# Kernel optimization log

Hardware: AMD Instinct MI355X
Metric: run time of the kernel (lower is better)

Reference implementation:

```python
import jax, jax.numpy as jnp
import numpy as np

N = 100000        # nodes
E = 1600000       # edges (avg degree 16)
IN_CH = 128
HID = 64
NUM_CLASSES = 40
LAYERS = 15
DT = 0.1
JACOBI_STEPS = 2


def setup_inputs() -> dict:
    key = jax.random.key(0)
    ks = jax.random.split(key, 8)
    x = jax.random.normal(ks[0], (N, IN_CH), dtype=jnp.float32)
    edge_index = jax.random.randint(ks[1], (2, E), 0, N, dtype=jnp.int32)
    s = 1.0 / np.sqrt(IN_CH)
    W_lx = jax.random.normal(ks[2], (IN_CH, HID), dtype=jnp.float32) * s
    b_lx = jnp.zeros((HID,), dtype=jnp.float32)
    W_ly = jax.random.normal(ks[3], (IN_CH, HID), dtype=jnp.float32) * s
    b_ly = jnp.zeros((HID,), dtype=jnp.float32)
    taus = jnp.full((LAYERS,), 0.7, dtype=jnp.float32)
    logit_scale = jnp.asarray(2.5, dtype=jnp.float32)
    W_ro = jax.random.normal(ks[4], (HID, NUM_CLASSES), dtype=jnp.float32) * (1.0 / np.sqrt(HID))
    b_ro = jnp.zeros((NUM_CLASSES,), dtype=jnp.float32)
    return {"x": x, "W_lx": W_lx, "b_lx": b_lx, "W_ly": W_ly, "b_ly": b_ly,
            "taus": taus, "logit_scale": logit_scale, "W_ro": W_ro, "b_ro": b_ro,
            "edge_index": edge_index}


def reference(x, W_lx, b_lx, W_ly, b_ly, taus, logit_scale, W_ro, b_ro, edge_index):
    # Eval mode: dropout is identity. y0_mode='ones' so lift_y is unused.
    src, dst = edge_index[0], edge_index[1]
    # symmetric normalization D^-1/2 A D^-1/2 from edge list
    deg = jax.ops.segment_sum(jnp.ones((E,), dtype=x.dtype), dst, num_segments=N)
    dinv = jax.lax.rsqrt(jnp.maximum(deg, 1.0))
    enorm = dinv[src] * dinv[dst]              # [E]

    def agg(Z):                                 # A_hat @ Z  via gather/scatter
        return jax.ops.segment_sum(enorm[:, None] * Z[src], dst, num_segments=N)

    X0 = jnp.tanh(x @ W_lx + b_lx)              # [N, HID]
    Y0 = jnp.ones_like(X0)
    h = jnp.concatenate([X0, Y0], axis=-1)      # [N, 2*HID]

    for l in range(LAYERS):
        X, Y = h[:, :HID], h[:, HID:]
        # Lotka-Volterra reaction terms
        fX = X * (1.0 - Y)
        fY = Y * (X - 1.0)
        rhs = jnp.concatenate([X + DT * fX, Y + DT * fY], axis=-1)
        # semi-implicit diffusion: ((1+dt)I - dt*A_hat) Z = rhs, Jacobi iterations
        Z = rhs
        for _ in range(JACOBI_STEPS):
            Z = (rhs + DT * agg(Z)) / (1.0 + DT)
        tau = jax.nn.sigmoid(taus[l])
        h = (1.0 - tau) * h + tau * Z

    Xout = h[:, :HID]
    return (logit_scale * Xout) @ W_ro + b_ro   # [N, NUM_CLASSES]
```

## Files before the change

### kernel.cpp

```cpp
#include <hip/hip_runtime.h>

#define DT_C   0.1f
#define INV1P  0.9090909090909091f


__device__ __forceinline__ unsigned bf16rne(float f) {
  unsigned b = __float_as_uint(f);
  return (b + 0x7fffu + ((b >> 16) & 1u)) >> 16;
}
__device__ __forceinline__ unsigned packbf(float x, float y) {
  return bf16rne(x) | (bf16rne(y) << 16);
}


#if __has_builtin(__builtin_amdgcn_cvt_pk_fp8_f32) && __has_builtin(__builtin_amdgcn_cvt_pk_f32_fp8)
typedef float vf2 __attribute__((ext_vector_type(2)));
__device__ __forceinline__ unsigned pk4_fp8(float a, float b, float c, float d) {
  int v = __builtin_amdgcn_cvt_pk_fp8_f32(a, b, 0, false);
  v = __builtin_amdgcn_cvt_pk_fp8_f32(c, d, v, true);
  return (unsigned)v;
}
__device__ __forceinline__ void unpk4_fp8(unsigned v, float& a, float& b, float& c, float& d) {
  vf2 lo = __builtin_amdgcn_cvt_pk_f32_fp8((int)v, false);
  vf2 hi = __builtin_amdgcn_cvt_pk_f32_fp8((int)v, true);
  a = lo[0]; b = lo[1]; c = hi[0]; d = hi[1];
}
#else
__device__ __forceinline__ unsigned enc8(float f) {
  unsigned u = __float_as_uint(f);
  unsigned mag = u & 0x7fffffffu;
  if (mag > 0x43E00000u) mag = 0x43E00000u;
  unsigned r = mag + 0x7FFFFu + ((mag >> 20) & 1u);
  int e8 = (int)(r >> 23) - 120;
  unsigned code = 0;
  if (e8 > 0) code = ((unsigned)(e8 > 15 ? 15 : e8) << 3) | ((r >> 20) & 7u);
  return code | ((u >> 24) & 0x80u);
}
__device__ __forceinline__ float dec8(unsigned c) {
  unsigned e = (c >> 3) & 15u, m = c & 7u, s = (c & 0x80u) << 24;
  if (e == 0) return __uint_as_float(s);
  return __uint_as_float(s | ((e + 120u) << 23) | (m << 20));
}
__device__ __forceinline__ unsigned pk4_fp8(float a, float b, float c, float d) {
  return enc8(a) | (enc8(b) << 8) | (enc8(c) << 16) | (enc8(d) << 24);
}
__device__ __forceinline__ void unpk4_fp8(unsigned v, float& a, float& b, float& c, float& d) {
  a = dec8(v & 0xffu); b = dec8((v >> 8) & 0xffu);
  c = dec8((v >> 16) & 0xffu); d = dec8(v >> 24);
}
#endif


__global__ __launch_bounds__(256) void k_deg(const int* __restrict__ dst,
                                             int* __restrict__ deg, int e) {
  int i = blockIdx.x * 256 + threadIdx.x;
  if (i < e) atomicAdd(&deg[dst[i]], 1);
}

__global__ __launch_bounds__(256) void k_dinv(const int* __restrict__ deg,
                                              float* __restrict__ dinv, int n) {
  int i = blockIdx.x * 256 + threadIdx.x;
  if (i < n) {
    float d = (float)deg[i];
    dinv[i] = rsqrtf(fmaxf(d, 1.0f));
  }
}

__global__ __launch_bounds__(1024) void k_scanA(const int* __restrict__ deg,
                                                int* __restrict__ rowptr,
                                                int* __restrict__ bsum, int n) {
  __shared__ int sm[1024];
  int t = threadIdx.x;
  int i = blockIdx.x * 1024 + t;
  int v = (i < n) ? deg[i] : 0;
  sm[t] = v;
  __syncthreads();
  for (int off = 1; off < 1024; off <<= 1) {
    int u = (t >= off) ? sm[t - off] : 0;
    __syncthreads();
    sm[t] += u;
    __syncthreads();
  }
  if (i < n) rowptr[i] = sm[t] - v;
  if (t == 1023) bsum[blockIdx.x] = sm[t];
}

__global__ __launch_bounds__(1024) void k_scanB(int* __restrict__ bsum, int g) {
  __shared__ int sm[1024];
  int t = threadIdx.x;
  int v = (t < g) ? bsum[t] : 0;
  sm[t] = v;
  __syncthreads();
  for (int off = 1; off < 1024; off <<= 1) {
    int u = (t >= off) ? sm[t - off] : 0;
    __syncthreads();
    sm[t] += u;
    __syncthreads();
  }
  if (t < g) bsum[t] = sm[t] - v;
}

__global__ __launch_bounds__(1024) void k_scanC(int* __restrict__ rowptr,
                                                const int* __restrict__ bsum,
                                                int n, int etot) {
  int i = blockIdx.x * 1024 + threadIdx.x;
  if (i < n) rowptr[i] += bsum[blockIdx.x];
  if (i == 0) rowptr[n] = etot;
}

__global__ __launch_bounds__(256) void k_fill(const int* __restrict__ src,
                                              const int* __restrict__ dst,
                                              const int* __restrict__ rowptr,
                                              int* __restrict__ deg,
                                              const float* __restrict__ dinv,
                                              unsigned* __restrict__ csr, int e) {
  int i = blockIdx.x * 256 + threadIdx.x;
  if (i >= e) return;
  int s = src[i], d = dst[i];
  int pos = rowptr[d] + atomicSub(&deg[d], 1) - 1;
  unsigned wb = __float_as_uint(dinv[s] * dinv[d]);
  wb = (wb + 0x10000u) & 0xFFFE0000u;
  csr[pos] = wb | (unsigned)s;
}


__global__ __launch_bounds__(256) void k_gemm_in(const float* __restrict__ x,
                                                 const float* __restrict__ Wlx,
                                                 const float* __restrict__ blx,
                                                 unsigned* __restrict__ h_b,
                                                 unsigned* __restrict__ rhs8,
                                                 int n, int ntiles) {
  __shared__ float xs[16 * 128];
  int t = threadIdx.x;
  int lane = t & 63;
  int wib  = t >> 6;
  unsigned wp[64];
#pragma unroll
  for (int j = 0; j < 64; ++j)
    wp[j] = packbf(Wlx[(2 * j) * 64 + lane], Wlx[(2 * j + 1) * 64 + lane]);
  float bl = blx[lane];

  for (int tile = blockIdx.x; tile < ntiles; tile += gridDim.x) {
    int base = tile * 16;
    __syncthreads();
    for (int v = t; v < 512; v += 256) {
      long idx = (long)base * 128 + v * 4;
      float4 val = {0.f, 0.f, 0.f, 0.f};
      if (idx < (long)n * 128) val = *(const float4*)(x + idx);
      *(float4*)(xs + v * 4) = val;
    }
    __syncthreads();
    for (int r = 0; r < 4; ++r) {
      int row = base + wib * 4 + r;
      if (row < n) {
        const float* xr = &xs[(wib * 4 + r) * 128];
        float acc = bl;
#pragma unroll
        for (int j = 0; j < 32; ++j) {
          float4 xv = *(const float4*)(xr + j * 4);
          unsigned p0 = wp[2 * j], p1 = wp[2 * j + 1];
          acc = fmaf(xv.x, __uint_as_float(p0 << 16),         acc);
          acc = fmaf(xv.y, __uint_as_float(p0 & 0xffff0000u), acc);
          acc = fmaf(xv.z, __uint_as_float(p1 << 16),         acc);
          acc = fmaf(xv.w, __uint_as_float(p1 & 0xffff0000u), acc);
        }
        float X0 = tanhf(acc);
        float a = __shfl(X0, (2 * lane) & 63);
        float b = __shfl(X0, (2 * lane + 1) & 63);
        unsigned hw = (lane < 32) ? packbf(a, b) : 0x3f803f80u;
        h_b[(size_t)row * 64 + lane] = hw;
        int b4 = (lane < 16) ? 4 * lane : 4 * (lane - 16);
        float v0 = __shfl(X0, (b4 + 0) & 63);
        float v1 = __shfl(X0, (b4 + 1) & 63);
        float v2 = __shfl(X0, (b4 + 2) & 63);
        float v3 = __shfl(X0, (b4 + 3) & 63);
        if (lane >= 16) {
          v0 = 1.f + DT_C * (v0 - 1.f);
          v1 = 1.f + DT_C * (v1 - 1.f);
          v2 = 1.f + DT_C * (v2 - 1.f);
          v3 = 1.f + DT_C * (v3 - 1.f);
        }
        unsigned pw = pk4_fp8(v0, v1, v2, v3);
        if (lane < 32) rhs8[(size_t)row * 32 + lane] = pw;
      }
    }
  }
}


__device__ __forceinline__ void rch_from_h(const unsigned hw[4], int q,
                                           float hv[8], float rch[8]) {
#pragma unroll
  for (int i = 0; i < 4; ++i) {
    hv[2 * i]     = __uint_as_float(hw[i] << 16);
    hv[2 * i + 1] = __uint_as_float(hw[i] & 0xffff0000u);
  }
  float pv[8];
#pragma unroll
  for (int i = 0; i < 8; ++i) pv[i] = __shfl_xor(hv[i], 8);
  bool isX = (q < 8);
#pragma unroll
  for (int i = 0; i < 8; ++i)
    rch[i] = isX ? hv[i] + DT_C * hv[i] * (1.0f - pv[i])
                 : hv[i] + DT_C * hv[i] * (pv[i] - 1.0f);
}

__device__ __forceinline__ void gather8(const unsigned* __restrict__ Zb8,
                                        const unsigned* __restrict__ csr,
                                        int beg, int end, int g, int q,
                                        float acc[8]) {
#pragma unroll
  for (int i = 0; i < 8; ++i) acc[i] = 0.f;
  int last = end - 1;
  const uint2* Z2 = (const uint2*)Zb8;
  for (int e0 = beg; e0 < end; e0 += 16) {
    unsigned c[4]; float wk[4]; uint2 u[4];
#pragma unroll
    for (int k = 0; k < 4; ++k) {
      int idx = e0 + 4 * k + g;
      int ic  = (idx < end) ? idx : last;
      c[k]  = csr[ic];
      wk[k] = (idx < end) ? __uint_as_float(c[k] & 0xFFFE0000u) : 0.f;
    }
#pragma unroll
    for (int k = 0; k < 4; ++k)
      u[k] = Z2[(size_t)(c[k] & 0x1FFFFu) * 16 + q];
#pragma unroll
    for (int k = 0; k < 4; ++k) {
      float f0, f1, f2, f3, f4, f5, f6, f7;
      unpk4_fp8(u[k].x, f0, f1, f2, f3);
      unpk4_fp8(u[k].y, f4, f5, f6, f7);
      acc[0] = fmaf(wk[k], f0, acc[0]);
      acc[1] = fmaf(wk[k], f1, acc[1]);
      acc[2] = fmaf(wk[k], f2, acc[2]);
      acc[3] = fmaf(wk[k], f3, acc[3]);
      acc[4] = fmaf(wk[k], f4, acc[4]);
      acc[5] = fmaf(wk[k], f5, acc[5]);
      acc[6] = fmaf(wk[k], f6, acc[6]);
      acc[7] = fmaf(wk[k], f7, acc[7]);
    }
  }
#pragma unroll
  for (int i = 0; i < 8; ++i) {
    acc[i] += __shfl_xor(acc[i], 16);
    acc[i] += __shfl_xor(acc[i], 32);
  }
}


__global__ __launch_bounds__(256) void k_aggA(const unsigned* __restrict__ rhs8,
                                              unsigned* __restrict__ Z18,
                                              const unsigned* __restrict__ h_b,
                                              const int* __restrict__ rowptr,
                                              const unsigned* __restrict__ csr, int n) {
  int node = __builtin_amdgcn_readfirstlane((blockIdx.x * 256 + threadIdx.x) >> 6);
  if (node >= n) return;
  int lane = threadIdx.x & 63;
  int g = lane >> 4, q = lane & 15;
  int beg = __builtin_amdgcn_readfirstlane(rowptr[node]);
  int end = __builtin_amdgcn_readfirstlane(rowptr[node + 1]);

  uint4 hb = *((const uint4*)(h_b + (size_t)node * 64) + q);
  unsigned hw[4] = {hb.x, hb.y, hb.z, hb.w};
  float hv[8], rch[8];
  rch_from_h(hw, q, hv, rch);

  float acc[8];
  gather8(rhs8, csr, beg, end, g, q, acc);

  float z[8];
#pragma unroll
  for (int i = 0; i < 8; ++i) z[i] = (rch[i] + DT_C * acc[i]) * INV1P;
  if (g == 0) {
    uint2 o;
    o.x = pk4_fp8(z[0], z[1], z[2], z[3]);
    o.y = pk4_fp8(z[4], z[5], z[6], z[7]);
    ((uint2*)Z18)[(size_t)node * 16 + q] = o;
  }
}


__global__ __launch_bounds__(256) void k_aggB(const unsigned* __restrict__ Z18,
                                              unsigned* __restrict__ rhs8,
                                              unsigned* __restrict__ h_b,
                                              const int* __restrict__ rowptr,
                                              const unsigned* __restrict__ csr,
                                              const float* __restrict__ taus,
                                              int layer, int n) {
  int node = __builtin_amdgcn_readfirstlane((blockIdx.x * 256 + threadIdx.x) >> 6);
  if (node >= n) return;
  int lane = threadIdx.x & 63;
  int g = lane >> 4, q = lane & 15;
  int beg = __builtin_amdgcn_readfirstlane(rowptr[node]);
  int end = __builtin_amdgcn_readfirstlane(rowptr[node + 1]);

  uint4 hb = *((const uint4*)(h_b + (size_t)node * 64) + q);
  unsigned hw[4] = {hb.x, hb.y, hb.z, hb.w};
  float hv[8], rch[8];
  rch_from_h(hw, q, hv, rch);

  float acc[8];
  gather8(Z18, csr, beg, end, g, q, acc);

  float tv  = taus[layer];
  float tau = 1.0f / (1.0f + expf(-tv));
  float hnew[8];
#pragma unroll
  for (int i = 0; i < 8; ++i) {
    float z = (rch[i] + DT_C * acc[i]) * INV1P;
    hnew[i] = (1.0f - tau) * hv[i] + tau * z;
  }
  if (g == 0) {
    uint4 o;
    o.x = packbf(hnew[0], hnew[1]);
    o.y = packbf(hnew[2], hnew[3]);
    o.z = packbf(hnew[4], hnew[5]);
    o.w = packbf(hnew[6], hnew[7]);
    *((uint4*)(h_b + (size_t)node * 64) + q) = o;
  }
  float pn[8];
#pragma unroll
  for (int i = 0; i < 8; ++i) pn[i] = __shfl_xor(hnew[i], 8);
  bool isX = (q < 8);
  float rn[8];
#pragma unroll
  for (int i = 0; i < 8; ++i)
    rn[i] = isX ? hnew[i] + DT_C * hnew[i] * (1.0f - pn[i])
                : hnew[i] + DT_C * hnew[i] * (pn[i] - 1.0f);
  if (g == 0) {
    uint2 o;
    o.x = pk4_fp8(rn[0], rn[1], rn[2], rn[3]);
    o.y = pk4_fp8(rn[4], rn[5], rn[6], rn[7]);
    ((uint2*)rhs8)[(size_t)node * 16 + q] = o;
  }
}


__global__ __launch_bounds__(256) void k_gemm_out(const unsigned* __restrict__ h_b,
                                                  const float* __restrict__ Wro,
                                                  const float* __restrict__ bro,
                                                  const float* __restrict__ lscale,
                                                  float* __restrict__ out, int n) {
  __shared__ float ws[64 * 40];
  __shared__ float xs[16 * 64];
  int t = threadIdx.x;
  for (int i = t; i < 64 * 40; i += 256) ws[i] = Wro[i];
  int base = blockIdx.x * 16;
  for (int v = t; v < 512; v += 256) {
    int rr = v >> 5;
    int wq = v & 31;
    int row = base + rr;
    float a = 0.f, b = 0.f;
    if (row < n) {
      unsigned u = h_b[(size_t)row * 64 + wq];
      a = __uint_as_float(u << 16);
      b = __uint_as_float(u & 0xffff0000u);
    }
    xs[rr * 64 + 2 * wq]     = a;
    xs[rr * 64 + 2 * wq + 1] = b;
  }
  __syncthreads();
  float ls = *lscale;
  int lane = t & 63;
  int wib  = t >> 6;
  float bb = (lane < 40) ? bro[lane] : 0.f;
  for (int r = 0; r < 4; ++r) {
    int row = base + wib * 4 + r;
    if (row < n && lane < 40) {
      const float* xr = &xs[(wib * 4 + r) * 64];
      float acc = 0.f;
#pragma unroll
      for (int k = 0; k < 64; ++k) acc = fmaf(xr[k], ws[k * 40 + lane], acc);
      out[row * 40 + lane] = ls * acc + bb;
    }
  }
}


extern "C" void kernel_launch(void* const* d_in, const int* in_sizes, int n_in,
                              void* d_out, int out_size, void* d_ws, size_t ws_size,
                              hipStream_t stream) {
  const float* x     = (const float*)d_in[0];
  const float* Wlx   = (const float*)d_in[1];
  const float* blx   = (const float*)d_in[2];
  const float* taus  = (const float*)d_in[5];
  const float* lsc   = (const float*)d_in[6];
  const float* Wro   = (const float*)d_in[7];
  const float* bro   = (const float*)d_in[8];
  const int*   eidx  = (const int*)d_in[9];
  int n = in_sizes[0] / 128;
  int e = in_sizes[9] / 2;
  const int* srcp = eidx;
  const int* dstp = eidx + e;
  float* out = (float*)d_out;

  char* ws = (char*)d_ws;
  size_t off = 0;
  auto alloc = [&](size_t bytes) -> void* {
    void* p = ws + off;
    off += (bytes + 255) & ~(size_t)255;
    return p;
  };
  int*      deg     = (int*)     alloc((size_t)n * 4);
  float*    dinv    = (float*)   alloc((size_t)n * 4);
  int*      rowptr  = (int*)     alloc((size_t)(n + 1) * 4);
  int*      bsum    = (int*)     alloc(1024 * 4);
  unsigned* csr     = (unsigned*)alloc((size_t)e * 4);
  unsigned* h_b     = (unsigned*)alloc((size_t)n * 64 * 4);
  unsigned* rhs8    = (unsigned*)alloc((size_t)n * 32 * 4);
  unsigned* Z18     = (unsigned*)alloc((size_t)n * 32 * 4);
  (void)ws_size; (void)n_in; (void)out_size;

  (void)hipMemsetAsync(deg, 0, (size_t)n * 4, stream);

  int eb = (e + 255) / 256;
  int sb = (n + 1023) / 1024;
  k_deg <<<eb, 256, 0, stream>>>(dstp, deg, e);
  k_dinv<<<(n + 255) / 256, 256, 0, stream>>>(deg, dinv, n);
  k_scanA<<<sb, 1024, 0, stream>>>(deg, rowptr, bsum, n);
  k_scanB<<<1, 1024, 0, stream>>>(bsum, sb);
  k_scanC<<<sb, 1024, 0, stream>>>(rowptr, bsum, n, e);
  k_fill<<<eb, 256, 0, stream>>>(srcp, dstp, rowptr, deg, dinv, csr, e);

  int ntiles = (n + 15) / 16;
  int gb = ntiles < 2048 ? ntiles : 2048;
  k_gemm_in<<<gb, 256, 0, stream>>>(x, Wlx, blx, h_b, rhs8, n, ntiles);

  int ab = (n * 64 + 255) / 256;
  for (int l = 0; l < 15; ++l) {
    k_aggA<<<ab, 256, 0, stream>>>(rhs8, Z18, h_b, rowptr, csr, n);
    k_aggB<<<ab, 256, 0, stream>>>(Z18, rhs8, h_b, rowptr, csr, taus, l, n);
  }

  k_gemm_out<<<(n + 15) / 16, 256, 0, stream>>>(h_b, Wro, bro, lsc, out, n);
}
```

Before: 1.691 ms.

## Process two nodes per wavefront in aggregation and drop h_b read in aggA

Each wavefront now handles two adjacent CSR rows in both Jacobi aggregation kernels, interleaving their edge gathers to raise memory-level parallelism. The first Jacobi kernel takes the right-hand side from the fp8 rhs buffer instead of recomputing it from bf16 h, removing one read of the state. The input GEMM is restructured to one wave per row, using lane shuffles instead of LDS staging. Costs are more registers per thread, fewer waves, and slightly different rounding in the first Jacobi step.

```diff
diff --git a/kernel.cpp b/kernel.cpp
--- a/kernel.cpp
+++ b/kernel.cpp
@@ -128,68 +128,159 @@
                                                  const float* __restrict__ Wlx,
                                                  const float* __restrict__ blx,
                                                  unsigned* __restrict__ h_b,
-                                                 unsigned* __restrict__ rhs8,
-                                                 int n, int ntiles) {
-  __shared__ float xs[16 * 128];
-  int t = threadIdx.x;
+                                                 unsigned* __restrict__ rhs8, int n) {
+  int t = blockIdx.x * 256 + threadIdx.x;
   int lane = t & 63;
-  int wib  = t >> 6;
+  int wid  = t >> 6;
+  int nW   = (gridDim.x * 256) >> 6;
   unsigned wp[64];
 #pragma unroll
   for (int j = 0; j < 64; ++j)
     wp[j] = packbf(Wlx[(2 * j) * 64 + lane], Wlx[(2 * j + 1) * 64 + lane]);
   float bl = blx[lane];
 
-  for (int tile = blockIdx.x; tile < ntiles; tile += gridDim.x) {
-    int base = tile * 16;
-    __syncthreads();
-    for (int v = t; v < 512; v += 256) {
-      long idx = (long)base * 128 + v * 4;
-      float4 val = {0.f, 0.f, 0.f, 0.f};
-      if (idx < (long)n * 128) val = *(const float4*)(x + idx);
-      *(float4*)(xs + v * 4) = val;
-    }
-    __syncthreads();
-    for (int r = 0; r < 4; ++r) {
-      int row = base + wib * 4 + r;
-      if (row < n) {
-        const float* xr = &xs[(wib * 4 + r) * 128];
-        float acc = bl;
-#pragma unroll
-        for (int j = 0; j < 32; ++j) {
-          float4 xv = *(const float4*)(xr + j * 4);
-          unsigned p0 = wp[2 * j], p1 = wp[2 * j + 1];
-          acc = fmaf(xv.x, __uint_as_float(p0 << 16),         acc);
-          acc = fmaf(xv.y, __uint_as_float(p0 & 0xffff0000u), acc);
-          acc = fmaf(xv.z, __uint_as_float(p1 << 16),         acc);
-          acc = fmaf(xv.w, __uint_as_float(p1 & 0xffff0000u), acc);
-        }
-        float X0 = tanhf(acc);
-        float a = __shfl(X0, (2 * lane) & 63);
-        float b = __shfl(X0, (2 * lane + 1) & 63);
-        unsigned hw = (lane < 32) ? packbf(a, b) : 0x3f803f80u;
-        h_b[(size_t)row * 64 + lane] = hw;
-        int b4 = (lane < 16) ? 4 * lane : 4 * (lane - 16);
-        float v0 = __shfl(X0, (b4 + 0) & 63);
-        float v1 = __shfl(X0, (b4 + 1) & 63);
-        float v2 = __shfl(X0, (b4 + 2) & 63);
-        float v3 = __shfl(X0, (b4 + 3) & 63);
-        if (lane >= 16) {
-          v0 = 1.f + DT_C * (v0 - 1.f);
-          v1 = 1.f + DT_C * (v1 - 1.f);
-          v2 = 1.f + DT_C * (v2 - 1.f);
-          v3 = 1.f + DT_C * (v3 - 1.f);
-        }
-        unsigned pw = pk4_fp8(v0, v1, v2, v3);
-        if (lane < 32) rhs8[(size_t)row * 32 + lane] = pw;
+  for (int row = wid; row < n; row += nW) {
+    float2 xv = *(const float2*)(x + (size_t)row * 128 + 2 * lane);
+    float acc = bl;
+#pragma unroll
+    for (int k = 0; k < 64; ++k) {
+      float bx = __shfl(xv.x, k);
+      float by = __shfl(xv.y, k);
+      acc = fmaf(bx, __uint_as_float(wp[k] << 16),         acc);
+      acc = fmaf(by, __uint_as_float(wp[k] & 0xffff0000u), acc);
+    }
+    float X0 = tanhf(acc);
+    float a = __shfl(X0, (2 * lane) & 63);
+    float b = __shfl(X0, (2 * lane + 1) & 63);
+    unsigned hw = (lane < 32) ? packbf(a, b) : 0x3f803f80u;
+    h_b[(size_t)row * 64 + lane] = hw;
+    int b4 = (lane < 16) ? 4 * lane : 4 * (lane - 16);
+    float v0 = __shfl(X0, (b4 + 0) & 63);
+    float v1 = __shfl(X0, (b4 + 1) & 63);
+    float v2 = __shfl(X0, (b4 + 2) & 63);
+    float v3 = __shfl(X0, (b4 + 3) & 63);
+    if (lane >= 16) {
+      v0 = 1.f + DT_C * (v0 - 1.f);
+      v1 = 1.f + DT_C * (v1 - 1.f);
+      v2 = 1.f + DT_C * (v2 - 1.f);
+      v3 = 1.f + DT_C * (v3 - 1.f);
+    }
+    unsigned pw = pk4_fp8(v0, v1, v2, v3);
+    if (lane < 32) rhs8[(size_t)row * 32 + lane] = pw;
+  }
+}
+
+
+__device__ __forceinline__ void batch_fma(const unsigned c[4], const float wk[4],
+                                          const uint2 u[4], float acc[8]) {
+#pragma unroll
+  for (int k = 0; k < 4; ++k) {
+    float f0, f1, f2, f3, f4, f5, f6, f7;
+    unpk4_fp8(u[k].x, f0, f1, f2, f3);
+    unpk4_fp8(u[k].y, f4, f5, f6, f7);
+    acc[0] = fmaf(wk[k], f0, acc[0]);
+    acc[1] = fmaf(wk[k], f1, acc[1]);
+    acc[2] = fmaf(wk[k], f2, acc[2]);
+    acc[3] = fmaf(wk[k], f3, acc[3]);
+    acc[4] = fmaf(wk[k], f4, acc[4]);
+    acc[5] = fmaf(wk[k], f5, acc[5]);
+    acc[6] = fmaf(wk[k], f6, acc[6]);
+    acc[7] = fmaf(wk[k], f7, acc[7]);
+  }
+}
+
+
+__global__ __launch_bounds__(256) void k_aggA(const unsigned* __restrict__ rhs8,
+                                              unsigned* __restrict__ Z18,
+                                              const int* __restrict__ rowptr,
+                                              const unsigned* __restrict__ csr, int n) {
+  int pair = __builtin_amdgcn_readfirstlane((blockIdx.x * 256 + threadIdx.x) >> 6);
+  int nodeA = 2 * pair;
+  if (nodeA >= n) return;
+  int nodeB = nodeA + 1;
+  bool hasB = nodeB < n;
+  int lane = threadIdx.x & 63;
+  int g = lane >> 4, q = lane & 15;
+  int begA = __builtin_amdgcn_readfirstlane(rowptr[nodeA]);
+  int endA = __builtin_amdgcn_readfirstlane(rowptr[nodeA + 1]);
+  int begB = endA;
+  int endB = hasB ? __builtin_amdgcn_readfirstlane(rowptr[nodeB + 1]) : begB;
+
+  const uint2* Z2 = (const uint2*)rhs8;
+  uint2 ra = Z2[(size_t)nodeA * 16 + q];
+  uint2 rb = hasB ? Z2[(size_t)nodeB * 16 + q] : ra;
+
+  float accA[8] = {0, 0, 0, 0, 0, 0, 0, 0};
+  float accB[8] = {0, 0, 0, 0, 0, 0, 0, 0};
+  int lastA = endA - 1, lastB = endB - 1;
+  for (int eA = begA, eB = begB; (eA < endA) || (eB < endB); eA += 16, eB += 16) {
+    bool doA = eA < endA, doB = eB < endB;
+    unsigned cA[4], cB[4]; float wA[4], wB[4]; uint2 uA[4], uB[4];
+    if (doA) {
+#pragma unroll
+      for (int k = 0; k < 4; ++k) {
+        int idx = eA + 4 * k + g;
+        int ic  = (idx < endA) ? idx : lastA;
+        cA[k] = csr[ic];
+        wA[k] = (idx < endA) ? __uint_as_float(cA[k] & 0xFFFE0000u) : 0.f;
       }
     }
-  }
-}
-
-
-__device__ __forceinline__ void rch_from_h(const unsigned hw[4], int q,
+    if (doB) {
+#pragma unroll
+      for (int k = 0; k < 4; ++k) {
+        int idx = eB + 4 * k + g;
+        int ic  = (idx < endB) ? idx : lastB;
+        cB[k] = csr[ic];
+        wB[k] = (idx < endB) ? __uint_as_float(cB[k] & 0xFFFE0000u) : 0.f;
+      }
+    }
+    if (doA) {
+#pragma unroll
+      for (int k = 0; k < 4; ++k) uA[k] = Z2[(size_t)(cA[k] & 0x1FFFFu) * 16 + q];
+    }
+    if (doB) {
+#pragma unroll
+      for (int k = 0; k < 4; ++k) uB[k] = Z2[(size_t)(cB[k] & 0x1FFFFu) * 16 + q];
+    }
+    if (doA) batch_fma(cA, wA, uA, accA);
+    if (doB) batch_fma(cB, wB, uB, accB);
+  }
+#pragma unroll
+  for (int i = 0; i < 8; ++i) {
+    accA[i] += __shfl_xor(accA[i], 16);
+    accA[i] += __shfl_xor(accA[i], 32);
+    accB[i] += __shfl_xor(accB[i], 16);
+    accB[i] += __shfl_xor(accB[i], 32);
+  }
+  float r8[8];
+  unpk4_fp8(ra.x, r8[0], r8[1], r8[2], r8[3]);
+  unpk4_fp8(ra.y, r8[4], r8[5], r8[6], r8[7]);
+  if (g == 0) {
+    uint2 o;
+    o.x = pk4_fp8((r8[0] + DT_C * accA[0]) * INV1P, (r8[1] + DT_C * accA[1]) * INV1P,
+                  (r8[2] + DT_C * accA[2]) * INV1P, (r8[3] + DT_C * accA[3]) * INV1P);
+    o.y = pk4_fp8((r8[4] + DT_C * accA[4]) * INV1P, (r8[5] + DT_C * accA[5]) * INV1P,
+                  (r8[6] + DT_C * accA[6]) * INV1P, (r8[7] + DT_C * accA[7]) * INV1P);
+    ((uint2*)Z18)[(size_t)nodeA * 16 + q] = o;
+  }
+  if (hasB) {
+    unpk4_fp8(rb.x, r8[0], r8[1], r8[2], r8[3]);
+    unpk4_fp8(rb.y, r8[4], r8[5], r8[6], r8[7]);
+    if (g == 0) {
+      uint2 o;
+      o.x = pk4_fp8((r8[0] + DT_C * accB[0]) * INV1P, (r8[1] + DT_C * accB[1]) * INV1P,
+                    (r8[2] + DT_C * accB[2]) * INV1P, (r8[3] + DT_C * accB[3]) * INV1P);
+      o.y = pk4_fp8((r8[4] + DT_C * accB[4]) * INV1P, (r8[5] + DT_C * accB[5]) * INV1P,
+                    (r8[6] + DT_C * accB[6]) * INV1P, (r8[7] + DT_C * accB[7]) * INV1P);
+      ((uint2*)Z18)[(size_t)nodeB * 16 + q] = o;
+    }
+  }
+}
+
+
+__device__ __forceinline__ void rch_from_h(const uint4 hb, int q,
                                            float hv[8], float rch[8]) {
+  unsigned hw[4] = {hb.x, hb.y, hb.z, hb.w};
 #pragma unroll
   for (int i = 0; i < 4; ++i) {
     hv[2 * i]     = __uint_as_float(hw[i] << 16);
@@ -205,105 +296,10 @@
                  : hv[i] + DT_C * hv[i] * (pv[i] - 1.0f);
 }
 
-__device__ __forceinline__ void gather8(const unsigned* __restrict__ Zb8,
-                                        const unsigned* __restrict__ csr,
-                                        int beg, int end, int g, int q,
-                                        float acc[8]) {
-#pragma unroll
-  for (int i = 0; i < 8; ++i) acc[i] = 0.f;
-  int last = end - 1;
-  const uint2* Z2 = (const uint2*)Zb8;
-  for (int e0 = beg; e0 < end; e0 += 16) {
-    unsigned c[4]; float wk[4]; uint2 u[4];
-#pragma unroll
-    for (int k = 0; k < 4; ++k) {
-      int idx = e0 + 4 * k + g;
-      int ic  = (idx < end) ? idx : last;
-      c[k]  = csr[ic];
-      wk[k] = (idx < end) ? __uint_as_float(c[k] & 0xFFFE0000u) : 0.f;
-    }
-#pragma unroll
-    for (int k = 0; k < 4; ++k)
-      u[k] = Z2[(size_t)(c[k] & 0x1FFFFu) * 16 + q];
-#pragma unroll
-    for (int k = 0; k < 4; ++k) {
-      float f0, f1, f2, f3, f4, f5, f6, f7;
-      unpk4_fp8(u[k].x, f0, f1, f2, f3);
-      unpk4_fp8(u[k].y, f4, f5, f6, f7);
-      acc[0] = fmaf(wk[k], f0, acc[0]);
-      acc[1] = fmaf(wk[k], f1, acc[1]);
-      acc[2] = fmaf(wk[k], f2, acc[2]);
-      acc[3] = fmaf(wk[k], f3, acc[3]);
-      acc[4] = fmaf(wk[k], f4, acc[4]);
-      acc[5] = fmaf(wk[k], f5, acc[5]);
-      acc[6] = fmaf(wk[k], f6, acc[6]);
-      acc[7] = fmaf(wk[k], f7, acc[7]);
-    }
-  }
-#pragma unroll
-  for (int i = 0; i < 8; ++i) {
-    acc[i] += __shfl_xor(acc[i], 16);
-    acc[i] += __shfl_xor(acc[i], 32);
-  }
-}
-
-
-__global__ __launch_bounds__(256) void k_aggA(const unsigned* __restrict__ rhs8,
-                                              unsigned* __restrict__ Z18,
-                                              const unsigned* __restrict__ h_b,
-                                              const int* __restrict__ rowptr,
-                                              const unsigned* __restrict__ csr, int n) {
-  int node = __builtin_amdgcn_readfirstlane((blockIdx.x * 256 + threadIdx.x) >> 6);
-  if (node >= n) return;
-  int lane = threadIdx.x & 63;
-  int g = lane >> 4, q = lane & 15;
-  int beg = __builtin_amdgcn_readfirstlane(rowptr[node]);
-  int end = __builtin_amdgcn_readfirstlane(rowptr[node + 1]);
-
-  uint4 hb = *((const uint4*)(h_b + (size_t)node * 64) + q);
-  unsigned hw[4] = {hb.x, hb.y, hb.z, hb.w};
-  float hv[8], rch[8];
-  rch_from_h(hw, q, hv, rch);
-
-  float acc[8];
-  gather8(rhs8, csr, beg, end, g, q, acc);
-
-  float z[8];
-#pragma unroll
-  for (int i = 0; i < 8; ++i) z[i] = (rch[i] + DT_C * acc[i]) * INV1P;
-  if (g == 0) {
-    uint2 o;
-    o.x = pk4_fp8(z[0], z[1], z[2], z[3]);
-    o.y = pk4_fp8(z[4], z[5], z[6], z[7]);
-    ((uint2*)Z18)[(size_t)node * 16 + q] = o;
-  }
-}
-
-
-__global__ __launch_bounds__(256) void k_aggB(const unsigned* __restrict__ Z18,
-                                              unsigned* __restrict__ rhs8,
-                                              unsigned* __restrict__ h_b,
-                                              const int* __restrict__ rowptr,
-                                              const unsigned* __restrict__ csr,
-                                              const float* __restrict__ taus,
-                                              int layer, int n) {
-  int node = __builtin_amdgcn_readfirstlane((blockIdx.x * 256 + threadIdx.x) >> 6);
-  if (node >= n) return;
-  int lane = threadIdx.x & 63;
-  int g = lane >> 4, q = lane & 15;
-  int beg = __builtin_amdgcn_readfirstlane(rowptr[node]);
-  int end = __builtin_amdgcn_readfirstlane(rowptr[node + 1]);
-
-  uint4 hb = *((const uint4*)(h_b + (size_t)node * 64) + q);
-  unsigned hw[4] = {hb.x, hb.y, hb.z, hb.w};
-  float hv[8], rch[8];
-  rch_from_h(hw, q, hv, rch);
-
-  float acc[8];
-  gather8(Z18, csr, beg, end, g, q, acc);
-
-  float tv  = taus[layer];
-  float tau = 1.0f / (1.0f + expf(-tv));
+__device__ __forceinline__ void finishB(const float hv[8], const float rch[8],
+                                        const float acc[8], float tau, int q, int g,
+                                        unsigned* __restrict__ h_b,
+                                        unsigned* __restrict__ rhs8, int node) {
   float hnew[8];
 #pragma unroll
   for (int i = 0; i < 8; ++i) {
@@ -333,6 +329,82 @@
     o.y = pk4_fp8(rn[4], rn[5], rn[6], rn[7]);
     ((uint2*)rhs8)[(size_t)node * 16 + q] = o;
   }
+}
+
+
+__global__ __launch_bounds__(256) void k_aggB(const unsigned* __restrict__ Z18,
+                                              unsigned* __restrict__ rhs8,
+                                              unsigned* __restrict__ h_b,
+                                              const int* __restrict__ rowptr,
+                                              const unsigned* __restrict__ csr,
+                                              const float* __restrict__ taus,
+                                              int layer, int n) {
+  int pair = __builtin_amdgcn_readfirstlane((blockIdx.x * 256 + threadIdx.x) >> 6);
+  int nodeA = 2 * pair;
+  if (nodeA >= n) return;
+  int nodeB = nodeA + 1;
+  bool hasB = nodeB < n;
+  int lane = threadIdx.x & 63;
+  int g = lane >> 4, q = lane & 15;
+  int begA = __builtin_amdgcn_readfirstlane(rowptr[nodeA]);
+  int endA = __builtin_amdgcn_readfirstlane(rowptr[nodeA + 1]);
+  int begB = endA;
+  int endB = hasB ? __builtin_amdgcn_readfirstlane(rowptr[nodeB + 1]) : begB;
+
+  uint4 hbA = *((const uint4*)(h_b + (size_t)nodeA * 64) + q);
+  uint4 hbB = hasB ? *((const uint4*)(h_b + (size_t)nodeB * 64) + q) : hbA;
+  float hvA[8], rchA[8], hvB[8], rchB[8];
+  rch_from_h(hbA, q, hvA, rchA);
+  rch_from_h(hbB, q, hvB, rchB);
+
+  const uint2* Z2 = (const uint2*)Z18;
+  float accA[8] = {0, 0, 0, 0, 0, 0, 0, 0};
+  float accB[8] = {0, 0, 0, 0, 0, 0, 0, 0};
+  int lastA = endA - 1, lastB = endB - 1;
+  for (int eA = begA, eB = begB; (eA < endA) || (eB < endB); eA += 16, eB += 16) {
+    bool doA = eA < endA, doB = eB < endB;
+    unsigned cA[4], cB[4]; float wA[4], wB[4]; uint2 uA[4], uB[4];
+    if (doA) {
+#pragma unroll
+      for (int k = 0; k < 4; ++k) {
+        int idx = eA + 4 * k + g;
+        int ic  = (idx < endA) ? idx : lastA;
+        cA[k] = csr[ic];
+        wA[k] = (idx < endA) ? __uint_as_float(cA[k] & 0xFFFE0000u) : 0.f;
+      }
+    }
+    if (doB) {
+#pragma unroll
+      for (int k = 0; k < 4; ++k) {
+        int idx = eB + 4 * k + g;
+        int ic  = (idx < endB) ? idx : lastB;
+        cB[k] = csr[ic];
+        wB[k] = (idx < endB) ? __uint_as_float(cB[k] & 0xFFFE0000u) : 0.f;
+      }
+    }
+    if (doA) {
+#pragma unroll
+      for (int k = 0; k < 4; ++k) uA[k] = Z2[(size_t)(cA[k] & 0x1FFFFu) * 16 + q];
+    }
+    if (doB) {
+#pragma unroll
+      for (int k = 0; k < 4; ++k) uB[k] = Z2[(size_t)(cB[k] & 0x1FFFFu) * 16 + q];
+    }
+    if (doA) batch_fma(cA, wA, uA, accA);
+    if (doB) batch_fma(cB, wB, uB, accB);
+  }
+#pragma unroll
+  for (int i = 0; i < 8; ++i) {
+    accA[i] += __shfl_xor(accA[i], 16);
+    accA[i] += __shfl_xor(accA[i], 32);
+    accB[i] += __shfl_xor(accB[i], 16);
+    accB[i] += __shfl_xor(accB[i], 32);
+  }
+
+  float tv  = taus[layer];
+  float tau = 1.0f / (1.0f + expf(-tv));
+  finishB(hvA, rchA, accA, tau, q, g, h_b, rhs8, nodeA);
+  if (hasB) finishB(hvB, rchB, accB, tau, q, g, h_b, rhs8, nodeB);
 }
 
 
@@ -422,13 +494,12 @@
   k_scanC<<<sb, 1024, 0, stream>>>(rowptr, bsum, n, e);
   k_fill<<<eb, 256, 0, stream>>>(srcp, dstp, rowptr, deg, dinv, csr, e);
 
-  int ntiles = (n + 15) / 16;
-  int gb = ntiles < 2048 ? ntiles : 2048;
-  k_gemm_in<<<gb, 256, 0, stream>>>(x, Wlx, blx, h_b, rhs8, n, ntiles);
-
-  int ab = (n * 64 + 255) / 256;
+  k_gemm_in<<<1024, 256, 0, stream>>>(x, Wlx, blx, h_b, rhs8, n);
+
+  int pairs = (n + 1) / 2;
+  int ab = (pairs * 64 + 255) / 256;
   for (int l = 0; l < 15; ++l) {
-    k_aggA<<<ab, 256, 0, stream>>>(rhs8, Z18, h_b, rowptr, csr, n);
+    k_aggA<<<ab, 256, 0, stream>>>(rhs8, Z18, rowptr, csr, n);
     k_aggB<<<ab, 256, 0, stream>>>(Z18, rhs8, h_b, rowptr, csr, taus, l, n);
   }
 
```

Result: slower. 2.273 ms (+34.4%).
